# Optimization experiments

Hardware: AMD Instinct MI355X
Metric: run time of the kernel (lower is better)

Reference implementation:

```python
import jax, jax.numpy as jnp
import numpy as np

B, C, H, W = 8, 64, 96, 320
K = 50
HEAD = 256
CLS = 3
CIN3 = C + 2 + CLS  # feat + 2 coord maps + one-hot class


def _conv(x, w, b, pad):
    y = jax.lax.conv_general_dilated(x, w, (1, 1), [(pad, pad), (pad, pad)],
                                     dimension_numbers=('NCHW', 'OIHW', 'NCHW'))
    return y + b[None, :, None, None]


def _head2(x, w1, b1, w2, b2):
    # Conv3x3 -> ReLU -> Conv1x1 (heatmap / offset_2d / size_2d heads)
    return _conv(jax.nn.relu(_conv(x, w1, b1, 1)), w2, b2, 0)


def _head3(x, w1, b1, g, be, m, v, w2, b2):
    # Conv3x3 -> BN(eval) -> ReLU -> AdaptiveAvgPool2d(1) -> Conv1x1, returns [N, cout]
    y = _conv(x, w1, b1, 1)
    y = (y - m[None, :, None, None]) * (g * jax.lax.rsqrt(v + 1e-5))[None, :, None, None] + be[None, :, None, None]
    y = jax.nn.relu(y).mean((2, 3))
    return y @ w2.reshape(w2.shape[0], -1).T + b2


def _nms(heat):
    hmax = jax.lax.reduce_window(heat, -jnp.inf, jax.lax.max, (1, 1, 3, 3), (1, 1, 1, 1), 'SAME')
    return jnp.where(hmax == heat, heat, 0.0)


def _roi_align(feat, boxes, out=7, sr=2):
    # torchvision roi_align semantics (spatial_scale=1, aligned=False, sampling_ratio=2);
    # boxes are treated as constants w.r.t. gradients (as in torchvision).
    boxes = jax.lax.stop_gradient(boxes)
    b = boxes[:, 0].astype(jnp.int32)
    x1, y1, x2, y2 = boxes[:, 1], boxes[:, 2], boxes[:, 3], boxes[:, 4]
    bw = jnp.maximum(x2 - x1, 1.0) / out
    bh = jnp.maximum(y2 - y1, 1.0) / out
    g = (jnp.arange(out * sr, dtype=feat.dtype) + 0.5) / sr  # sample positions in bin units
    ys = y1[:, None] + g[None, :] * bh[:, None]  # [N, S]
    xs = x1[:, None] + g[None, :] * bw[:, None]
    Hf, Wf = feat.shape[2], feat.shape[3]
    def prep(c, dim):
        valid = (c >= -1.0) & (c <= dim)
        c = jnp.clip(c, 0.0, dim - 1.0)
        i0 = jnp.floor(c).astype(jnp.int32)
        i1 = jnp.minimum(i0 + 1, dim - 1)
        return i0, i1, c - i0, valid
    y0, y1i, fy, vy = prep(ys, Hf)
    x0, x1i, fx, vx = prep(xs, Wf)
    bb = b[:, None, None]
    def gather(yi, xi):
        return feat[bb, :, yi[:, :, None], xi[:, None, :]]  # [N, S, S, C]
    w00 = ((1 - fy)[:, :, None] * (1 - fx)[:, None, :])[..., None]
    w01 = ((1 - fy)[:, :, None] * fx[:, None, :])[..., None]
    w10 = (fy[:, :, None] * (1 - fx)[:, None, :])[..., None]
    w11 = (fy[:, :, None] * fx[:, None, :])[..., None]
    val = gather(y0, x0) * w00 + gather(y0, x1i) * w01 + gather(y1i, x0) * w10 + gather(y1i, x1i) * w11
    val = val * (vy[:, :, None] & vx[:, None, :])[..., None].astype(feat.dtype)
    N = boxes.shape[0]
    val = val.reshape(N, out, sr, out, sr, -1).mean((2, 4))  # avg over sampling grid
    return val.transpose(0, 3, 1, 2)  # [N, C, 7, 7]


def _project2rect(calib, p):
    f_u, f_v = calib[:, 0, 0], calib[:, 1, 1]
    c_u, c_v = calib[:, 0, 2], calib[:, 1, 2]
    b_x = calib[:, 0, 3] / -f_u
    b_y = calib[:, 1, 3] / -f_v
    x = (p[:, 0] - c_u) * p[:, 2] / f_u + b_x
    y = (p[:, 1] - c_v) * p[:, 2] / f_v + b_y
    return jnp.stack([x, y, p[:, 2]], -1)


def reference(feat, coord_ranges, calibs, mean_size, hm_w1, hm_b1, hm_w2, hm_b2, o2_w1, o2_b1, o2_w2, o2_b2, s2_w1, s2_b1, s2_w2, s2_b2, dep_w1, dep_b1, dep_g, dep_be, dep_m, dep_v, dep_w2, dep_b2, o3_w1, o3_b1, o3_g, o3_be, o3_m, o3_v, o3_w2, o3_b2, s3_w1, s3_b1, s3_g, s3_be, s3_m, s3_v, s3_w2, s3_b2, hd_w1, hd_b1, hd_g, hd_be, hd_m, hd_v, hd_w2, hd_b2):
    # dense 2D heads
    heatmap = _head2(feat, hm_w1, hm_b1, hm_w2, hm_b2)        # [B,1,H,W]
    offset_2d = _head2(feat, o2_w1, o2_b1, o2_w2, o2_b2)      # [B,2,H,W]
    size_2d = _head2(feat, s2_w1, s2_b1, s2_w2, s2_b2)        # [B,2,H,W]
    # test-mode: NMS + topK (single-class heatmap -> cls ids all 0)
    heat = _nms(jnp.clip(jax.nn.sigmoid(heatmap), 1e-4, 1.0 - 1e-4))
    _, inds = jax.lax.top_k(heat.reshape(B, -1), K)           # [B,K]
    cls_flat = jnp.zeros((B * K,), jnp.int32)
    # box2d maps in feature coords
    xg = jnp.arange(W, dtype=feat.dtype)
    yg = jnp.arange(H, dtype=feat.dtype)
    coord_map = jnp.stack([jnp.broadcast_to(xg[None, :], (H, W)), jnp.broadcast_to(yg[:, None], (H, W))], 0)
    centre = coord_map[None] + offset_2d
    box2d = jnp.concatenate([centre - size_2d / 2, centre + size_2d / 2], 1)  # [B,4,H,W]
    bidx = jnp.broadcast_to(jnp.arange(B, dtype=feat.dtype)[:, None, None, None], (B, 1, H, W))
    bm = jnp.concatenate([bidx, box2d], 1).reshape(B, 5, H * W)
    boxes = jnp.take_along_axis(bm, inds[:, None, :], 2).transpose(0, 2, 1).reshape(B * K, 5)
    roi = _roi_align(feat, boxes)                             # [N,64,7,7]
    bsel = boxes[:, 0].astype(jnp.int32)
    cr = coord_ranges[bsel]
    sx = cr[:, 1, 0] - cr[:, 0, 0]
    sy = cr[:, 1, 1] - cr[:, 0, 1]
    boxes_r = jnp.stack([boxes[:, 0],
                         boxes[:, 1] / W * sx + cr[:, 0, 0],
                         boxes[:, 2] / H * sy + cr[:, 0, 1],
                         boxes[:, 3] / W * sx + cr[:, 0, 0],
                         boxes[:, 4] / H * sy + cr[:, 0, 1]], -1)
    roi_calibs = calibs[bsel]
    ones = jnp.ones((B * K, 1), feat.dtype)
    p1 = _project2rect(roi_calibs, jnp.concatenate([boxes_r[:, 1:3], ones], -1))[:, :2]
    p2 = _project2rect(roi_calibs, jnp.concatenate([boxes_r[:, 3:5], ones], -1))[:, :2]
    cam = jnp.concatenate([p1, p2], -1)                       # [N,4]
    t = jnp.arange(7, dtype=feat.dtype) / 6.0
    xs7 = cam[:, 0:1] + t[None, :] * (cam[:, 2:3] - cam[:, 0:1])
    ys7 = cam[:, 1:2] + t[None, :] * (cam[:, 3:4] - cam[:, 1:2])
    cmx = jnp.broadcast_to(xs7[:, None, None, :], (B * K, 1, 7, 7))
    cmy = jnp.broadcast_to(ys7[:, None, :, None], (B * K, 1, 7, 7))
    hots = jax.nn.one_hot(cls_flat, CLS, dtype=feat.dtype)
    roi_full = jnp.concatenate([roi, cmx, cmy, jnp.broadcast_to(hots[:, :, None, None], (B * K, CLS, 7, 7))], 1)
    h2d = jnp.maximum(boxes_r[:, 4] - boxes_r[:, 2], 1.0)
    s3 = _head3(roi_full, s3_w1, s3_b1, s3_g, s3_be, s3_m, s3_v, s3_w2, s3_b2)  # [N,4]
    h3d_log_std = s3[:, 3:4]
    size3d_offset = s3[:, :3]
    size_3d = mean_size[cls_flat] + size3d_offset
    f_u = roi_calibs[:, 0, 0]
    depth_geo = size_3d[:, 0] / h2d * f_u
    dno = _head3(roi_full, dep_w1, dep_b1, dep_g, dep_be, dep_m, dep_v, dep_w2, dep_b2)  # [N,2]
    geo_log_std = (h3d_log_std[:, 0] + 2.0 * (jnp.log(f_u) - jnp.log(h2d)))[:, None]
    net_log_std = jax.nn.logsumexp(jnp.concatenate([dno[:, 1:2], geo_log_std], -1), -1, keepdims=True)
    depth = jnp.concatenate([1.0 / (jax.nn.sigmoid(dno[:, 0:1]) + 1e-6) - 1.0 + depth_geo[:, None], net_log_std], -1)
    heading = _head3(roi_full, hd_w1, hd_b1, hd_g, hd_be, hd_m, hd_v, hd_w2, hd_b2)
    offset_3d = _head3(roi_full, o3_w1, o3_b1, o3_g, o3_be, o3_m, o3_v, o3_w2, o3_b2)
    return (heatmap, offset_2d, size_2d, heading, depth, offset_3d, size3d_offset, h3d_log_std)


def setup_inputs() -> dict:
    keys = iter(jax.random.split(jax.random.key(0), 40))
    def rn(shape, s=0.05):
        return jax.random.normal(next(keys), shape, jnp.float32) * s
    d = {}
    d['feat'] = jax.random.normal(next(keys), (B, C, H, W), jnp.float32)
    d['coord_ranges'] = jnp.tile(jnp.array([[0.0, 0.0], [1280.0, 384.0]], jnp.float32)[None], (B, 1, 1))
    d['calibs'] = jnp.tile(jnp.array([[720.0, 0.0, 640.0, 0.04], [0.0, 720.0, 190.0, 0.01], [0.0, 0.0, 1.0, 0.003]], jnp.float32)[None], (B, 1, 1))
    d['mean_size'] = jnp.array([[1.52, 1.63, 3.88], [1.73, 0.67, 0.88], [1.77, 0.60, 1.76]], jnp.float32)
    for pfx, cout in [('hm', 1), ('o2', 2), ('s2', 2)]:
        d[pfx + '_w1'] = rn((HEAD, C, 3, 3))
        d[pfx + '_b1'] = jnp.zeros((HEAD,), jnp.float32)
        d[pfx + '_w2'] = rn((cout, HEAD, 1, 1))
        d[pfx + '_b2'] = jnp.full((cout,), -2.19, jnp.float32) if pfx == 'hm' else jnp.zeros((cout,), jnp.float32)
    for pfx, cout in [('dep', 2), ('o3', 2), ('s3', 4), ('hd', 24)]:
        d[pfx + '_w1'] = rn((HEAD, CIN3, 3, 3))
        d[pfx + '_b1'] = jnp.zeros((HEAD,), jnp.float32)
        d[pfx + '_g'] = jnp.ones((HEAD,), jnp.float32)
        d[pfx + '_be'] = jnp.zeros((HEAD,), jnp.float32)
        d[pfx + '_m'] = jnp.zeros((HEAD,), jnp.float32)
        d[pfx + '_v'] = jnp.ones((HEAD,), jnp.float32)
        d[pfx + '_w2'] = rn((cout, HEAD, 1, 1))
        d[pfx + '_b2'] = jnp.zeros((cout,), jnp.float32)
    return d
```

## Files before the change

kernel.cpp:

```cpp
#include <hip/hip_runtime.h>


constexpr int OFF_O2    = 245760;
constexpr int OFF_S2    = 737280;
constexpr int OFF_HEAD  = 1228800;
constexpr int OFF_DEPTH = 1238400;
constexpr int OFF_O3D   = 1239200;
constexpr int OFF_S3D   = 1240000;
constexpr int OFF_H3D   = 1241200;

constexpr int WS_W1T  = 0;
constexpr int WS_BNSC = 635904;
constexpr int WS_BNSH = 636928;
constexpr int WS_KEEP = 637952;
constexpr int WS_INDS = 883712;
constexpr int WS_BOX  = 884112;
constexpr int WS_XS7  = 885712;
constexpr int WS_YS7  = 888512;
constexpr int WS_FU   = 891312;
constexpr int WS_H2D  = 891712;
constexpr int WS_DNO  = 892112;
constexpr int WS_ROIF = 892912;
constexpr int WS_SIG  = WS_ROIF;
constexpr int WS_W1R  = 2245312;
constexpr int WS_WPACK2 = 2245312;
constexpr int WS_FEATH  = 2540224;
constexpr int WS_FEATL  = 10618560;
constexpr long long FAST_REQ_BYTES = 18696896LL * 4;
constexpr int WS_WPACK3 = 18696896;
constexpr int WS_A3     = 19139264;
constexpr long long FAST3_REQ_BYTES = 20694464LL * 4;

typedef __attribute__((ext_vector_type(4))) float f32x4;
typedef __attribute__((ext_vector_type(8))) _Float16 f16x8;
typedef __attribute__((ext_vector_type(4))) unsigned int u32x4;

__global__ void repack_kernel(
    const float* __restrict__ w2h, const float* __restrict__ w2o, const float* __restrict__ w2s,
    const float* __restrict__ w3d, const float* __restrict__ w3o, const float* __restrict__ w3s, const float* __restrict__ w3h,
    const float* __restrict__ g0, const float* __restrict__ be0, const float* __restrict__ m0, const float* __restrict__ v0,
    const float* __restrict__ g1, const float* __restrict__ be1, const float* __restrict__ m1, const float* __restrict__ v1,
    const float* __restrict__ g2, const float* __restrict__ be2, const float* __restrict__ m2, const float* __restrict__ v2,
    const float* __restrict__ g3, const float* __restrict__ be3, const float* __restrict__ m3, const float* __restrict__ v3,
    int skip2, int skip3, float* __restrict__ ws)
{
  int i = blockIdx.x * 256 + threadIdx.x;
  if (i < 3 * 147456) {
    if (skip2) return;
    int br = i / 147456, r = i - br * 147456, q = r >> 8, c = r & 255;
    const float* src = br == 0 ? w2h : (br == 1 ? w2o : w2s);
    ws[WS_W1R + i] = src[c * 576 + q];
  } else if (i < 3 * 147456 + 4 * 158976) {
    if (skip3) return;
    int j = i - 3 * 147456;
    int br = j / 158976, r = j - br * 158976, q = r >> 8, c = r & 255;
    const float* src = br == 0 ? w3d : (br == 1 ? w3o : (br == 2 ? w3s : w3h));
    ws[WS_W1T + j] = src[c * 621 + q];
  } else {
    int j = i - (3 * 147456 + 4 * 158976);
    if (j < 1024) {
      int br = j >> 8, c = j & 255;
      const float* g  = br == 0 ? g0  : (br == 1 ? g1  : (br == 2 ? g2  : g3));
      const float* be = br == 0 ? be0 : (br == 1 ? be1 : (br == 2 ? be2 : be3));
      const float* m  = br == 0 ? m0  : (br == 1 ? m1  : (br == 2 ? m2  : m3));
      const float* v  = br == 0 ? v0  : (br == 1 ? v1  : (br == 2 ? v2  : v3));
      float sc = g[c] * rsqrtf(v[c] + 1e-5f);
      ws[WS_BNSC + j] = sc;
      ws[WS_BNSH + j] = be[c] - m[c] * sc;
    }
  }
}

__global__ void wpack2_kernel(const float* __restrict__ hm_w1, const float* __restrict__ o2_w1,
                              const float* __restrict__ s2_w1, float* __restrict__ ws)
{
  int i = blockIdx.x * 256 + threadIdx.x;
  if (i >= 4 * 18 * 256 * 32) return;
  int br = i / 147456; int r = i - br * 147456;
  int c = r / 8192; int r2 = r - c * 8192;
  int n = r2 >> 5; int kk = r2 & 31;
  int kg = c * 32 + kk;
  int tap = kg >> 6, ci = kg & 63;
  const float* w1 = (br == 0) ? o2_w1 : (br == 1 ? s2_w1 : hm_w1);
  float v = w1[n * 576 + ci * 9 + tap];
  _Float16 hi = (_Float16)v;
  _Float16 valh;
  if (br == 3) valh = (_Float16)(v - (float)hi);
  else valh = hi;
  unsigned short bits = __builtin_bit_cast(unsigned short, valh);
  long long didx = (((((long long)br * 18 + c) * 16 + (n >> 4)) * 4 + (kk >> 3)) * 128) + (n & 15) * 8 + (kk & 7);
  unsigned short* dst = (unsigned short*)(ws + WS_WPACK2);
  dst[didx] = bits;
}

__global__ void wpack3_kernel(const float* __restrict__ w3d, const float* __restrict__ w3o,
                              const float* __restrict__ w3s, const float* __restrict__ w3h,
                              float* __restrict__ ws)
{
  int i = blockIdx.x * 256 + threadIdx.x;
  if (i >= 4 * 27 * 256 * 32) return;
  int br = i / 221184; int r = i - br * 221184;
  int s = r / 8192; int r2 = r - s * 8192;
  int n = r2 >> 5; int kk = r2 & 31;
  int tap = s / 3; int cc = s - tap * 3;
  int ch = cc * 32 + kk;
  const float* w1 = br == 0 ? w3d : (br == 1 ? w3o : (br == 2 ? w3s : w3h));
  float v = (ch < 69) ? w1[n * 621 + ch * 9 + tap] : 0.f;
  unsigned short bits = __builtin_bit_cast(unsigned short, (_Float16)v);
  long long didx = (((((long long)br * 27 + s) * 16 + (n >> 4)) * 4 + (kk >> 3)) * 128) + (n & 15) * 8 + (kk & 7);
  ((unsigned short*)(ws + WS_WPACK3))[didx] = bits;
}

__global__ void pad_zero_kernel(float* __restrict__ ws)
{
  int i = blockIdx.x * 256 + threadIdx.x;
  if (i >= 428032) return;
  int arr = i / 214016; int r = i - arr * 214016;
  int px = r >> 5, q = r & 31;
  int b = px / 836, pr = px - b * 836;
  int yy, xx;
  if (pr < 322) { yy = 0; xx = pr; }
  else if (pr < 644) { yy = 97; xx = pr - 322; }
  else { int t = pr - 644; yy = 1 + (t >> 1); xx = (t & 1) * 321; }
  unsigned int* dst = (unsigned int*)(ws + (arr ? WS_FEATL : WS_FEATH));
  dst[((b * 98 + yy) * 322 + xx) * 32 + q] = 0u;
}

__global__ __launch_bounds__(256) void transpose_kernel(const float* __restrict__ feat, float* __restrict__ ws)
{
  __shared__ unsigned short T2[2][64 * 65];
  int bx = blockIdx.x;
  int b = bx / 480; int r = bx % 480; int y = r / 5; int x0 = (r % 5) * 64;
  int tid = threadIdx.x;
  int lx = tid & 63, grp = tid >> 6;
  #pragma unroll
  for (int it = 0; it < 16; ++it) {
    int ci = it * 4 + grp;
    float v = feat[(((b * 64 + ci) * 96 + y) * 320) + x0 + lx];
    _Float16 h = (_Float16)v;
    _Float16 l = (_Float16)(v - (float)h);
    T2[0][lx * 65 + ci] = __builtin_bit_cast(unsigned short, h);
    T2[1][lx * 65 + ci] = __builtin_bit_cast(unsigned short, l);
  }
  __syncthreads();
  unsigned int* fH = (unsigned int*)(ws + WS_FEATH);
  unsigned int* fL = (unsigned int*)(ws + WS_FEATL);
  #pragma unroll
  for (int it = 0; it < 16; ++it) {
    int unit = it * 256 + tid;
    int arr = unit >> 11; int un = unit & 2047;
    int x = un >> 5, pr = un & 31;
    unsigned int lo = T2[arr][x * 65 + pr * 2];
    unsigned int hi = T2[arr][x * 65 + pr * 2 + 1];
    unsigned int val = lo | (hi << 16);
    unsigned int* dst = arr ? fL : fH;
    dst[((b * 98 + y + 1) * 322 + (x0 + x + 1)) * 32 + pr] = val;
  }
}


__global__ __launch_bounds__(256, 2) void head2_os_kernel(
    const float* __restrict__ ws,
    const float* __restrict__ b1o, const float* __restrict__ b1s,
    const float* __restrict__ w2o, const float* __restrict__ w2s,
    const float* __restrict__ b2o, const float* __restrict__ b2s,
    float* __restrict__ out)
{
  __shared__ unsigned char tile[4 * 8 * 66 * 16];
  __shared__ float red[1024];
  const int tid = threadIdx.x;
  const int l = tid & 63, w = tid >> 6;
  const int bx = blockIdx.x;
  const int b = bx / 240; int r = bx % 240;
  const int y0 = (r / 5) * 2; const int x0 = (r % 5) * 64;
  const unsigned short* fH = (const unsigned short*)(ws + WS_FEATH) + (size_t)b * (98 * 322 * 64);
  const _Float16* wpk = (const _Float16*)(ws + WS_WPACK2);

  for (int t = 0; t < 9; ++t) {
    int u = t * 256 + tid;
    if (u < 2112) {
      int row = u / 528; int rem = u - row * 528;
      int j0 = rem / 66, x = rem - j0 * 66;
      u32x4 v = *(const u32x4*)(fH + ((y0 + row) * 322 + (x0 + x)) * 64 + j0 * 8);
      *(u32x4*)(tile + ((row * 8 + j0) * 66 + x) * 16) = v;
    }
  }
  __syncthreads();

  const int l15 = l & 15, lg = l >> 4;
  const int aBase = (lg * 66 + l15) * 16;

  #pragma unroll 1
  for (int br = 0; br < 2; ++br) {
    f32x4 acc[8][4];
    #pragma unroll
    for (int i = 0; i < 8; ++i)
      #pragma unroll
      for (int j = 0; j < 4; ++j) acc[i][j] = (f32x4)(0.f);

    const _Float16* wB = wpk + (((long long)(br * 18) * 16 + w * 4) * 4 + lg) * 128 + l15 * 8;

    #pragma unroll
    for (int s = 0; s < 18; ++s) {
      const int tap = s >> 1, half = s & 1;
      const int ky = tap / 3, kx = tap - ky * 3;
      const int stepOff = ((ky * 8 + half * 4) * 66 + kx) * 16;
      f16x8 af[8], bf[4];
      #pragma unroll
      for (int pf = 0; pf < 8; ++pf) {
        const int frOff = (pf < 4) ? pf * 256 : 8448 + (pf - 4) * 256;
        af[pf] = *(const f16x8*)(tile + aBase + frOff + stepOff);
      }
      #pragma unroll
      for (int nf = 0; nf < 4; ++nf)
        bf[nf] = *(const f16x8*)(wB + s * 8192 + nf * 512);
      #pragma unroll
      for (int pf = 0; pf < 8; ++pf)
        #pragma unroll
        for (int nf = 0; nf < 4; ++nf)
          acc[pf][nf] = __builtin_amdgcn_mfma_f32_16x16x32_f16(af[pf], bf[nf], acc[pf][nf], 0, 0, 0);
    }

    const float* b1 = br == 0 ? b1o : b1s;
    const float* w2 = br == 0 ? w2o : w2s;
    const float* b2 = br == 0 ? b2o : b2s;
    float b1v_[4], w2v[2][4];
    #pragma unroll
    for (int nf = 0; nf < 4; ++nf) {
      int n = w * 64 + nf * 16 + l15;
      b1v_[nf] = b1[n];
      w2v[0][nf] = w2[n];
      w2v[1][nf] = w2[256 + n];
    }
    __syncthreads();
    #pragma unroll
    for (int pf = 0; pf < 8; ++pf) {
      #pragma unroll
      for (int rr = 0; rr < 4; ++rr) {
        float s0 = 0.f, s1 = 0.f;
        #pragma unroll
        for (int nf = 0; nf < 4; ++nf) {
          float yv = acc[pf][nf][rr] + b1v_[nf];
          yv = yv > 0.f ? yv : 0.f;
          s0 = fmaf(w2v[0][nf], yv, s0);
          s1 = fmaf(w2v[1][nf], yv, s1);
        }
        #pragma unroll
        for (int m = 1; m < 16; m <<= 1) {
          s0 += __shfl_xor(s0, m);
          s1 += __shfl_xor(s1, m);
        }
        if (l15 == 0) {
          int p = pf * 16 + lg * 4 + rr;
          red[(w * 2 + 0) * 128 + p] = s0;
          red[(w * 2 + 1) * 128 + p] = s1;
        }
      }
    }
    __syncthreads();
    {
      int p = tid & 127, o = tid >> 7;
      float s = red[(0 * 2 + o) * 128 + p] + red[(1 * 2 + o) * 128 + p] +
                red[(2 * 2 + o) * 128 + p] + red[(3 * 2 + o) * 128 + p] + b2[o];
      int ypix = y0 + (p >> 6), xpix = x0 + (p & 63);
      int base = (br == 0) ? OFF_O2 : OFF_S2;
      out[base + ((b * 2 + o) * 96 + ypix) * 320 + xpix] = s;
    }
  }
}

__global__ __launch_bounds__(256, 2) void head2_hm_kernel(
    const float* __restrict__ ws,
    const float* __restrict__ b1h, const float* __restrict__ w2h, const float* __restrict__ b2h,
    float* __restrict__ out)
{
  __shared__ unsigned char tiles[2 * 3 * 8 * 66 * 16];
  __shared__ float red[256];
  const int tid = threadIdx.x;
  const int l = tid & 63, w = tid >> 6;
  const int bx = blockIdx.x;
  const int b = bx / 480; int r = bx % 480;
  const int y = r / 5; const int x0 = (r % 5) * 64;
  const unsigned short* fH = (const unsigned short*)(ws + WS_FEATH) + (size_t)b * (98 * 322 * 64);
  const unsigned short* fL = (const unsigned short*)(ws + WS_FEATL) + (size_t)b * (98 * 322 * 64);
  const _Float16* wpk = (const _Float16*)(ws + WS_WPACK2);

  for (int t = 0; t < 13; ++t) {
    int u = t * 256 + tid;
    if (u < 3168) {
      int arr = u >= 1584; int uu = u - arr * 1584;
      int row = uu / 528; int rem = uu - row * 528;
      int j0 = rem / 66, x = rem - j0 * 66;
      const unsigned short* src = arr ? fL : fH;
      u32x4 v = *(const u32x4*)(src + ((y + row) * 322 + (x0 + x)) * 64 + j0 * 8);
      *(u32x4*)(tiles + arr * 25344 + ((row * 8 + j0) * 66 + x) * 16) = v;
    }
  }
  __syncthreads();

  const int l15 = l & 15, lg = l >> 4;
  const int aBase = (lg * 66 + l15) * 16;

  f32x4 acc[4][4];
  #pragma unroll
  for (int i = 0; i < 4; ++i)
    #pragma unroll
    for (int j = 0; j < 4; ++j) acc[i][j] = (f32x4)(0.f);

  const _Float16* wBH = wpk + (((long long)(2 * 18) * 16 + w * 4) * 4 + lg) * 128 + l15 * 8;
  const _Float16* wBL = wpk + (((long long)(3 * 18) * 16 + w * 4) * 4 + lg) * 128 + l15 * 8;

  #pragma unroll
  for (int s = 0; s < 18; ++s) {
    const int tap = s >> 1, half = s & 1;
    const int ky = tap / 3, kx = tap - ky * 3;
    const int stepOff = ((ky * 8 + half * 4) * 66 + kx) * 16;
    f16x8 ah[4], al[4], bh[4], bl[4];
    #pragma unroll
    for (int pf = 0; pf < 4; ++pf) {
      ah[pf] = *(const f16x8*)(tiles + aBase + pf * 256 + stepOff);
      al[pf] = *(const f16x8*)(tiles + 25344 + aBase + pf * 256 + stepOff);
    }
    #pragma unroll
    for (int nf = 0; nf < 4; ++nf) {
      bh[nf] = *(const f16x8*)(wBH + s * 8192 + nf * 512);
      bl[nf] = *(const f16x8*)(wBL + s * 8192 + nf * 512);
    }
    #pragma unroll
    for (int pf = 0; pf < 4; ++pf)
      #pragma unroll
      for (int nf = 0; nf < 4; ++nf)
        acc[pf][nf] = __builtin_amdgcn_mfma_f32_16x16x32_f16(ah[pf], bh[nf], acc[pf][nf], 0, 0, 0);
    #pragma unroll
    for (int pf = 0; pf < 4; ++pf)
      #pragma unroll
      for (int nf = 0; nf < 4; ++nf)
        acc[pf][nf] = __builtin_amdgcn_mfma_f32_16x16x32_f16(ah[pf], bl[nf], acc[pf][nf], 0, 0, 0);
    #pragma unroll
    for (int pf = 0; pf < 4; ++pf)
      #pragma unroll
      for (int nf = 0; nf < 4; ++nf)
        acc[pf][nf] = __builtin_amdgcn_mfma_f32_16x16x32_f16(al[pf], bh[nf], acc[pf][nf], 0, 0, 0);
  }

  float b1v_[4], w2v[4];
  #pragma unroll
  for (int nf = 0; nf < 4; ++nf) {
    int n = w * 64 + nf * 16 + l15;
    b1v_[nf] = b1h[n];
    w2v[nf] = w2h[n];
  }
  __syncthreads();
  #pragma unroll
  for (int pf = 0; pf < 4; ++pf) {
    #pragma unroll
    for (int rr = 0; rr < 4; ++rr) {
      float s0 = 0.f;
      #pragma unroll
      for (int nf = 0; nf < 4; ++nf) {
        float yv = acc[pf][nf][rr] + b1v_[nf];
        yv = yv > 0.f ? yv : 0.f;
        s0 = fmaf(w2v[nf], yv, s0);
      }
      #pragma unroll
      for (int m = 1; m < 16; m <<= 1) s0 += __shfl_xor(s0, m);
      if (l15 == 0) red[w * 64 + pf * 16 + lg * 4 + rr] = s0;
    }
  }
  __syncthreads();
  if (tid < 64) {
    float s = red[tid] + red[64 + tid] + red[128 + tid] + red[192 + tid] + b2h[0];
    out[(b * 96 + y) * 320 + x0 + tid] = s;
  }
}

__global__ __launch_bounds__(256) void head2_kernel(
    const float* __restrict__ feat, const float* __restrict__ ws,
    const float* __restrict__ b1h, const float* __restrict__ b1o, const float* __restrict__ b1s,
    const float* __restrict__ w2h, const float* __restrict__ w2o, const float* __restrict__ w2s,
    const float* __restrict__ b2h, const float* __restrict__ b2o, const float* __restrict__ b2s,
    float* __restrict__ out)
{
  __shared__ float xs[32 * 10 * 34];
  const int tid = threadIdx.x;
  const int tx = tid & 31, ty = tid >> 5;
  const int x0 = blockIdx.x * 32, y0 = blockIdx.y * 8, bz = blockIdx.z;
  const int px = x0 + tx, py = y0 + ty;
  const float* w1r = ws + WS_W1R;

  #pragma unroll 1
  for (int br = 0; br < 3; ++br) {
    const float* wr = w1r + br * 147456;
    const float* b1 = br == 0 ? b1h : (br == 1 ? b1o : b1s);
    const float* w2 = br == 0 ? w2h : (br == 1 ? w2o : w2s);
    const int cout = (br == 0) ? 1 : 2;
    float acc0 = 0.f, acc1 = 0.f;
    #pragma unroll 1
    for (int c0 = 0; c0 < 256; c0 += 64) {
      float part[64];
      #pragma unroll
      for (int j = 0; j < 64; ++j) part[j] = 0.f;
      #pragma unroll 1
      for (int cc = 0; cc < 2; ++cc) {
        for (int i = tid; i < 32 * 10 * 34; i += 256) {
          int ci = i / 340; int rr = i - ci * 340; int ry = rr / 34; int rx = rr - ry * 34;
          int gy = y0 + ry - 1, gx = x0 + rx - 1;
          float v = 0.f;
          if ((unsigned)gy < 96u && (unsigned)gx < 320u)
            v = feat[((bz * 64 + cc * 32 + ci) * 96 + gy) * 320 + gx];
          xs[i] = v;
        }
        __syncthreads();
        #pragma unroll 1
        for (int ci = 0; ci < 32; ++ci) {
          const float* wp = wr + ((cc * 32 + ci) * 9) * 256 + c0;
          const float* xb = &xs[ci * 340 + ty * 34 + tx];
          #pragma unroll
          for (int k = 0; k < 9; ++k) {
            float xv = xb[(k / 3) * 34 + (k % 3)];
            const float* wk = wp + k * 256;
            #pragma unroll
            for (int j = 0; j < 64; ++j) part[j] = fmaf(wk[j], xv, part[j]);
          }
        }
        __syncthreads();
      }
      #pragma unroll
      for (int j = 0; j < 64; ++j) {
        float yv = part[j] + b1[c0 + j];
        yv = yv > 0.f ? yv : 0.f;
        acc0 = fmaf(w2[c0 + j], yv, acc0);
        if (cout > 1) acc1 = fmaf(w2[256 + c0 + j], yv, acc1);
      }
    }
    if (br == 0) {
      out[(bz * 96 + py) * 320 + px] = acc0 + b2h[0];
    } else if (br == 1) {
      out[OFF_O2 + ((bz * 2 + 0) * 96 + py) * 320 + px] = acc0 + b2o[0];
      out[OFF_O2 + ((bz * 2 + 1) * 96 + py) * 320 + px] = acc1 + b2o[1];
    } else {
      out[OFF_S2 + ((bz * 2 + 0) * 96 + py) * 320 + px] = acc0 + b2s[0];
      out[OFF_S2 + ((bz * 2 + 1) * 96 + py) * 320 + px] = acc1 + b2s[1];
    }
  }
}

__global__ void nms_sig_kernel(const float* __restrict__ out, float* __restrict__ sig)
{
  int i = blockIdx.x * 256 + threadIdx.x;
  if (i >= 8 * 30720) return;
  float s = 1.f / (1.f + expf(-out[i]));
  s = s < 1e-4f ? 1e-4f : s;
  float hi = 1.f - 1e-4f;
  sig[i] = s > hi ? hi : s;
}

__global__ void nms_max_kernel(const float* __restrict__ sig, float* __restrict__ keep)
{
  int i = blockIdx.x * 256 + threadIdx.x;
  if (i >= 8 * 30720) return;
  int b = i / 30720; int r = i - b * 30720; int y = r / 320; int x = r - y * 320;
  const float* sb = sig + b * 30720;
  float v = sb[y * 320 + x];
  float m = v;
  for (int dy = -1; dy <= 1; ++dy)
    for (int dx = -1; dx <= 1; ++dx) {
      int yy = y + dy, xx = x + dx;
      if (yy >= 0 && yy < 96 && xx >= 0 && xx < 320) m = fmaxf(m, sb[yy * 320 + xx]);
    }
  keep[i] = (m == v) ? v : 0.f;
}

__global__ __launch_bounds__(256) void topk_kernel(float* ws)
{
  constexpr int CAP = 6144;
  __shared__ float cv[CAP];
  __shared__ int   cix[CAP];
  __shared__ int   cnt;
  __shared__ float wv_[4];
  __shared__ int   wi_[4];
  __shared__ int   wsl[4];
  int b = blockIdx.x, tid = threadIdx.x;
  int lane = tid & 63, wid = tid >> 6;
  if (tid == 0) cnt = 0;
  __syncthreads();
  const float* kb = ws + WS_KEEP + b * 30720;
  for (int i = tid; i < 30720; i += 256) {
    float v = kb[i];
    if (v > 0.f) {
      int pos = atomicAdd(&cnt, 1);
      if (pos < CAP) { cv[pos] = v; cix[pos] = i; }
    }
  }
  __syncthreads();
  int ncand = cnt < CAP ? cnt : CAP;
  int* inds = (int*)(ws + WS_INDS);
  for (int k = 0; k < 50; ++k) {
    float bv = -1.f; int bi = 0x7fffffff; int bs = -1;
    for (int i = tid; i < ncand; i += 256) {
      float v = cv[i]; int id = cix[i];
      if (v > bv || (v == bv && id < bi)) { bv = v; bi = id; bs = i; }
    }
    #pragma unroll
    for (int m = 1; m < 64; m <<= 1) {
      float ov = __shfl_xor(bv, m);
      int oi = __shfl_xor(bi, m);
      int os_ = __shfl_xor(bs, m);
      if (ov > bv || (ov == bv && oi < bi)) { bv = ov; bi = oi; bs = os_; }
    }
    if (lane == 0) { wv_[wid] = bv; wi_[wid] = bi; wsl[wid] = bs; }
    __syncthreads();
    if (tid == 0) {
      float fv = wv_[0]; int fi = wi_[0]; int fs = wsl[0];
      #pragma unroll
      for (int t = 1; t < 4; ++t) {
        if (wv_[t] > fv || (wv_[t] == fv && wi_[t] < fi)) { fv = wv_[t]; fi = wi_[t]; fs = wsl[t]; }
      }
      inds[b * 50 + k] = fi;
      if (fs >= 0) cv[fs] = -1.f;
    }
    __syncthreads();
  }
}

__global__ void boxes_kernel(const float* __restrict__ out, const float* __restrict__ coord_ranges,
                             const float* __restrict__ calibs, float* ws)
{
  int n = blockIdx.x * 256 + threadIdx.x;
  if (n >= 400) return;
  const int* inds = (const int*)(ws + WS_INDS);
  int b = n / 50;
  int idx = inds[n];
  int iy = idx / 320, ix = idx - iy * 320;
  float o2x = out[OFF_O2 + ((b * 2 + 0) * 96 + iy) * 320 + ix];
  float o2y = out[OFF_O2 + ((b * 2 + 1) * 96 + iy) * 320 + ix];
  float sw  = out[OFF_S2 + ((b * 2 + 0) * 96 + iy) * 320 + ix];
  float sh  = out[OFF_S2 + ((b * 2 + 1) * 96 + iy) * 320 + ix];
  float cx = (float)ix + o2x, cy = (float)iy + o2y;
  float x1 = cx - sw * 0.5f, y1 = cy - sh * 0.5f, x2 = cx + sw * 0.5f, y2 = cy + sh * 0.5f;
  ws[WS_BOX + n * 4 + 0] = x1; ws[WS_BOX + n * 4 + 1] = y1;
  ws[WS_BOX + n * 4 + 2] = x2; ws[WS_BOX + n * 4 + 3] = y2;
  float cr00 = coord_ranges[b * 4 + 0], cr01 = coord_ranges[b * 4 + 1];
  float sx = coord_ranges[b * 4 + 2] - cr00, sy = coord_ranges[b * 4 + 3] - cr01;
  float x1r = x1 / 320.f * sx + cr00, y1r = y1 / 96.f * sy + cr01;
  float x2r = x2 / 320.f * sx + cr00, y2r = y2 / 96.f * sy + cr01;
  const float* cl = calibs + b * 12;
  float fu = cl[0], cu = cl[2], bx = cl[3] / (-fu);
  float fv = cl[5], cvv = cl[6], by = cl[7] / (-fv);
  float p1x = (x1r - cu) / fu + bx, p1y = (y1r - cvv) / fv + by;
  float p2x = (x2r - cu) / fu + bx, p2y = (y2r - cvv) / fv + by;
  #pragma unroll
  for (int j = 0; j < 7; ++j) {
    float t = (float)j / 6.f;
    ws[WS_XS7 + n * 7 + j] = p1x + t * (p2x - p1x);
    ws[WS_YS7 + n * 7 + j] = p1y + t * (p2y - p1y);
  }
  ws[WS_FU + n] = fu;
  ws[WS_H2D + n] = fmaxf(y2r - y1r, 1.f);
}

__global__ __launch_bounds__(256) void roi_kernel(const float* __restrict__ feat, float* ws)
{
  int n = blockIdx.x;
  int tid = threadIdx.x;
  __shared__ int   iy0[14], iy1[14], ix0[14], ix1[14];
  __shared__ float fy[14], fx[14], vy[14], vx[14];
  float bx1 = ws[WS_BOX + n * 4], by1 = ws[WS_BOX + n * 4 + 1];
  float bx2 = ws[WS_BOX + n * 4 + 2], by2 = ws[WS_BOX + n * 4 + 3];
  if (tid < 14) {
    float bh = fmaxf(by2 - by1, 1.f) / 7.f;
    float g = ((float)tid + 0.5f) * 0.5f;
    float c = by1 + g * bh;
    vy[tid] = (c >= -1.f && c <= 96.f) ? 1.f : 0.f;
    c = fminf(fmaxf(c, 0.f), 95.f);
    int i0 = (int)floorf(c);
    iy0[tid] = i0; iy1[tid] = (i0 + 1 < 95) ? i0 + 1 : 95;
    fy[tid] = c - (float)i0;
  } else if (tid < 28) {
    int t = tid - 14;
    float bw = fmaxf(bx2 - bx1, 1.f) / 7.f;
    float g = ((float)t + 0.5f) * 0.5f;
    float c = bx1 + g * bw;
    vx[t] = (c >= -1.f && c <= 320.f) ? 1.f : 0.f;
    c = fminf(fmaxf(c, 0.f), 319.f);
    int i0 = (int)floorf(c);
    ix0[t] = i0; ix1[t] = (i0 + 1 < 319) ? i0 + 1 : 319;
    fx[t] = c - (float)i0;
  }
  __syncthreads();
  int bsel = n / 50;
  const float* fbase = feat + bsel * 64 * 30720;
  float* rf = ws + WS_ROIF + n * 3381;
  for (int i = tid; i < 64 * 49; i += 256) {
    int c = i / 49, p = i - c * 49;
    int oy = p / 7, ox = p - oy * 7;
    const float* fb = fbase + c * 30720;
    float s = 0.f;
    #pragma unroll
    for (int sy2 = 0; sy2 < 2; ++sy2) {
      #pragma unroll
      for (int sx2 = 0; sx2 < 2; ++sx2) {
        int jy = oy * 2 + sy2, jx = ox * 2 + sx2;
        const float* r0 = fb + iy0[jy] * 320;
        const float* r1 = fb + iy1[jy] * 320;
        float gy = fy[jy], gx = fx[jx];
        float v00 = r0[ix0[jx]], v01 = r0[ix1[jx]], v10 = r1[ix0[jx]], v11 = r1[ix1[jx]];
        float v = v00 * (1.f - gy) * (1.f - gx) + v01 * (1.f - gy) * gx
                + v10 * gy * (1.f - gx) + v11 * gy * gx;
        s += v * vy[jy] * vx[jx];
      }
    }
    rf[c * 49 + p] = s * 0.25f;
  }
  if (tid < 5 * 49) {
    int ch = tid / 49, p = tid - ch * 49;
    int oy = p / 7, ox = p - oy * 7;
    float v;
    if (ch == 0) v = ws[WS_XS7 + n * 7 + ox];
    else if (ch == 1) v = ws[WS_YS7 + n * 7 + oy];
    else if (ch == 2) v = 1.f;
    else v = 0.f;
    rf[(64 + ch) * 49 + p] = v;
  }
}

__global__ void roi16_kernel(float* __restrict__ ws)
{
  int n = blockIdx.x;
  const float* rf = ws + WS_ROIF + n * 3381;
  unsigned short* a3 = (unsigned short*)(ws + WS_A3) + (size_t)n * 7776;
  for (int t = 0; t < 31; ++t) {
    int i = t * 256 + threadIdx.x;
    if (i < 7776) {
      int pr = i / 96, ch = i - pr * 96;
      int py = pr / 9, px = pr - py * 9;
      float v = 0.f;
      if (py >= 1 && py <= 7 && px >= 1 && px <= 7 && ch < 69)
        v = rf[ch * 49 + (py - 1) * 7 + (px - 1)];
      a3[i] = __builtin_bit_cast(unsigned short, (_Float16)v);
    }
  }
}

__global__ __launch_bounds__(256, 2) void head3m_kernel(
    float* __restrict__ ws,
    const float* __restrict__ b1d, const float* __restrict__ b1o3, const float* __restrict__ b1s3, const float* __restrict__ b1hd,
    const float* __restrict__ w2d, const float* __restrict__ w2o3, const float* __restrict__ w2s3, const float* __restrict__ w2hd,
    const float* __restrict__ b2d, const float* __restrict__ b2o3, const float* __restrict__ b2s3, const float* __restrict__ b2hd,
    float* __restrict__ out)
{
  __shared__ unsigned char A[81 * 104 * 2];
  __shared__ float ym[256];
  const int tid = threadIdx.x;
  const int l = tid & 63, w = tid >> 6;
  const int l15 = l & 15, lg = l >> 4;
  const int n = blockIdx.x;
  const unsigned short* a3 = (const unsigned short*)(ws + WS_A3) + (size_t)n * 7776;
  const _Float16* wp3 = (const _Float16*)(ws + WS_WPACK3);

  #pragma unroll
  for (int t = 0; t < 4; ++t) {
    int u = t * 256 + tid;
    if (u < 972) {
      int row = u / 12, cu = u - row * 12;
      u32x4 v = *(const u32x4*)(a3 + u * 8);
      *(u32x4*)(A + (row * 104 + cu * 8) * 2) = v;
    }
  }
  __syncthreads();

  int aB[4];
  #pragma unroll
  for (int pf = 0; pf < 4; ++pf) {
    int p = pf * 16 + l15;
    int rb = (p < 49) ? ((p / 7) * 9 + (p % 7)) : 0;
    aB[pf] = rb * 208 + lg * 16;
  }

  #pragma unroll 1
  for (int br = 0; br < 4; ++br) {
    const float* b1 = br == 0 ? b1d : (br == 1 ? b1o3 : (br == 2 ? b1s3 : b1hd));
    const float* w2 = br == 0 ? w2d : (br == 1 ? w2o3 : (br == 2 ? w2s3 : w2hd));
    const float* b2 = br == 0 ? b2d : (br == 1 ? b2o3 : (br == 2 ? b2s3 : b2hd));
    const int cout = br == 0 ? 2 : (br == 1 ? 2 : (br == 2 ? 4 : 24));

    f32x4 acc[4][4];
    #pragma unroll
    for (int i = 0; i < 4; ++i)
      #pragma unroll
      for (int j = 0; j < 4; ++j) acc[i][j] = (f32x4)(0.f);

    const _Float16* wB3 = wp3 + (((long long)(br * 27) * 16 + w * 4) * 4 + lg) * 128 + l15 * 8;

    #pragma unroll
    for (int s = 0; s < 27; ++s) {
      const int tap = s / 3, cc = s - tap * 3;
      const int ky = tap / 3, kx = tap - ky * 3;
      const int stepOff = (ky * 9 + kx) * 208 + cc * 64;
      f16x8 af[4], bf[4];
      #pragma unroll
      for (int pf = 0; pf < 4; ++pf)
        af[pf] = *(const f16x8*)(A + aB[pf] + stepOff);
      #pragma unroll
      for (int nf = 0; nf < 4; ++nf)
        bf[nf] = *(const f16x8*)(wB3 + s * 8192 + nf * 512);
      #pragma unroll
      for (int pf = 0; pf < 4; ++pf)
        #pragma unroll
        for (int nf = 0; nf < 4; ++nf)
          acc[pf][nf] = __builtin_amdgcn_mfma_f32_16x16x32_f16(af[pf], bf[nf], acc[pf][nf], 0, 0, 0);
    }

    #pragma unroll
    for (int nf = 0; nf < 4; ++nf) {
      int nn = w * 64 + nf * 16 + l15;
      float b1n = b1[nn];
      float scn = ws[WS_BNSC + br * 256 + nn];
      float shn = ws[WS_BNSH + br * 256 + nn];
      float local = 0.f;
      #pragma unroll
      for (int pf = 0; pf < 4; ++pf) {
        #pragma unroll
        for (int rr = 0; rr < 4; ++rr) {
          int p = pf * 16 + lg * 4 + rr;
          float yv = (acc[pf][nf][rr] + b1n) * scn + shn;
          yv = yv > 0.f ? yv : 0.f;
          local += (p < 49) ? yv : 0.f;
        }
      }
      local += __shfl_xor(local, 16);
      local += __shfl_xor(local, 32);
      if (lg == 0) ym[nn] = local;
    }
    __syncthreads();
    for (int o = w; o < cout; o += 4) {
      float p = 0.f;
      #pragma unroll
      for (int t = 0; t < 4; ++t) p = fmaf(w2[o * 256 + t * 64 + l], ym[t * 64 + l], p);
      p *= (1.f / 49.f);
      #pragma unroll
      for (int off = 32; off > 0; off >>= 1) p += __shfl_down(p, off);
      if (l == 0) {
        float v = p + b2[o];
        if (br == 0) ws[WS_DNO + n * 2 + o] = v;
        else if (br == 1) out[OFF_O3D + n * 2 + o] = v;
        else if (br == 2) { if (o < 3) out[OFF_S3D + n * 3 + o] = v; else out[OFF_H3D + n] = v; }
        else out[OFF_HEAD + n * 24 + o] = v;
      }
    }
    __syncthreads();
  }
}

__global__ __launch_bounds__(256) void head3_kernel(
    float* ws,
    const float* __restrict__ b1d, const float* __restrict__ b1o3, const float* __restrict__ b1s3, const float* __restrict__ b1hd,
    const float* __restrict__ w2d, const float* __restrict__ w2o3, const float* __restrict__ w2s3, const float* __restrict__ w2hd,
    const float* __restrict__ b2d, const float* __restrict__ b2o3, const float* __restrict__ b2s3, const float* __restrict__ b2hd,
    float* __restrict__ out)
{
  int n = blockIdx.x, br = blockIdx.y;
  int c = threadIdx.x;
  __shared__ float ym[256];
  const float* wt = ws + WS_W1T + br * 158976;
  const float* b1 = br == 0 ? b1d : (br == 1 ? b1o3 : (br == 2 ? b1s3 : b1hd));
  const float* w2 = br == 0 ? w2d : (br == 1 ? w2o3 : (br == 2 ? w2s3 : w2hd));
  const float* b2 = br == 0 ? b2d : (br == 1 ? b2o3 : (br == 2 ? b2s3 : b2hd));
  const int cout = br == 0 ? 2 : (br == 1 ? 2 : (br == 2 ? 4 : 24));
  const float* xin0 = ws + WS_ROIF + n * 3381;

  float acc[49];
  #pragma unroll
  for (int i = 0; i < 49; ++i) acc[i] = 0.f;

  #pragma unroll 1
  for (int ci = 0; ci < 69; ++ci) {
    float wv[9];
    #pragma unroll
    for (int k = 0; k < 9; ++k) wv[k] = wt[(ci * 9 + k) * 256 + c];
    const float* xin = xin0 + ci * 49;
    #pragma unroll
    for (int y = 0; y < 7; ++y) {
      float xr[9];
      xr[0] = 0.f; xr[8] = 0.f;
      #pragma unroll
      for (int q = 0; q < 7; ++q) xr[q + 1] = xin[y * 7 + q];
      #pragma unroll
      for (int ky = 0; ky < 3; ++ky) {
        int pyy = y + 1 - ky;
        if (pyy >= 0 && pyy < 7) {
          #pragma unroll
          for (int kx = 0; kx < 3; ++kx) {
            float w = wv[ky * 3 + kx];
            #pragma unroll
            for (int pxx = 0; pxx < 7; ++pxx)
              acc[pyy * 7 + pxx] = fmaf(w, xr[pxx + kx], acc[pyy * 7 + pxx]);
          }
        }
      }
    }
  }
  float b1c = b1[c];
  float sc = ws[WS_BNSC + br * 256 + c];
  float sh = ws[WS_BNSH + br * 256 + c];
  float sum = 0.f;
  #pragma unroll
  for (int i = 0; i < 49; ++i) {
    float yv = (acc[i] + b1c) * sc + sh;
    sum += yv > 0.f ? yv : 0.f;
  }
  ym[c] = sum / 49.f;
  __syncthreads();
  int lane = c & 63, wid = c >> 6;
  for (int o = wid; o < cout; o += 4) {
    float p = 0.f;
    #pragma unroll
    for (int t = 0; t < 4; ++t) p = fmaf(w2[o * 256 + t * 64 + lane], ym[t * 64 + lane], p);
    #pragma unroll
    for (int off = 32; off > 0; off >>= 1) p += __shfl_down(p, off);
    if (lane == 0) {
      float v = p + b2[o];
      if (br == 0) ws[WS_DNO + n * 2 + o] = v;
      else if (br == 1) out[OFF_O3D + n * 2 + o] = v;
      else if (br == 2) { if (o < 3) out[OFF_S3D + n * 3 + o] = v; else out[OFF_H3D + n] = v; }
      else out[OFF_HEAD + n * 24 + o] = v;
    }
  }
}

__global__ void depth_kernel(const float* ws, const float* __restrict__ mean_size, float* __restrict__ out)
{
  int n = blockIdx.x * 256 + threadIdx.x;
  if (n >= 400) return;
  float h3d = out[OFF_H3D + n];
  float s30 = out[OFF_S3D + n * 3];
  float size0 = mean_size[0] + s30;
  float f = ws[WS_FU + n], h = ws[WS_H2D + n];
  float dgeo = size0 / h * f;
  float geo = h3d + 2.f * (logf(f) - logf(h));
  float a = ws[WS_DNO + n * 2 + 1];
  float mx = fmaxf(a, geo);
  float nls = mx + logf(expf(a - mx) + expf(geo - mx));
  float sg = 1.f / (1.f + expf(-ws[WS_DNO + n * 2]));
  out[OFF_DEPTH + n * 2] = 1.f / (sg + 1e-6f) - 1.f + dgeo;
  out[OFF_DEPTH + n * 2 + 1] = nls;
}

extern "C" void kernel_launch(void* const* d_in, const int* in_sizes, int n_in,
                              void* d_out, int out_size, void* d_ws, size_t ws_size,
                              hipStream_t stream)
{
  const float* feat         = (const float*)d_in[0];
  const float* coord_ranges = (const float*)d_in[1];
  const float* calibs       = (const float*)d_in[2];
  const float* mean_size    = (const float*)d_in[3];
  const float* hm_w1 = (const float*)d_in[4];
  const float* hm_b1 = (const float*)d_in[5];
  const float* hm_w2 = (const float*)d_in[6];
  const float* hm_b2 = (const float*)d_in[7];
  const float* o2_w1 = (const float*)d_in[8];
  const float* o2_b1 = (const float*)d_in[9];
  const float* o2_w2 = (const float*)d_in[10];
  const float* o2_b2 = (const float*)d_in[11];
  const float* s2_w1 = (const float*)d_in[12];
  const float* s2_b1 = (const float*)d_in[13];
  const float* s2_w2 = (const float*)d_in[14];
  const float* s2_b2 = (const float*)d_in[15];
  const float* dep_w1 = (const float*)d_in[16];
  const float* dep_b1 = (const float*)d_in[17];
  const float* dep_g  = (const float*)d_in[18];
  const float* dep_be = (const float*)d_in[19];
  const float* dep_m  = (const float*)d_in[20];
  const float* dep_v  = (const float*)d_in[21];
  const float* dep_w2 = (const float*)d_in[22];
  const float* dep_b2 = (const float*)d_in[23];
  const float* o3_w1 = (const float*)d_in[24];
  const float* o3_b1 = (const float*)d_in[25];
  const float* o3_g  = (const float*)d_in[26];
  const float* o3_be = (const float*)d_in[27];
  const float* o3_m  = (const float*)d_in[28];
  const float* o3_v  = (const float*)d_in[29];
  const float* o3_w2 = (const float*)d_in[30];
  const float* o3_b2 = (const float*)d_in[31];
  const float* s3_w1 = (const float*)d_in[32];
  const float* s3_b1 = (const float*)d_in[33];
  const float* s3_g  = (const float*)d_in[34];
  const float* s3_be = (const float*)d_in[35];
  const float* s3_m  = (const float*)d_in[36];
  const float* s3_v  = (const float*)d_in[37];
  const float* s3_w2 = (const float*)d_in[38];
  const float* s3_b2 = (const float*)d_in[39];
  const float* hd_w1 = (const float*)d_in[40];
  const float* hd_b1 = (const float*)d_in[41];
  const float* hd_g  = (const float*)d_in[42];
  const float* hd_be = (const float*)d_in[43];
  const float* hd_m  = (const float*)d_in[44];
  const float* hd_v  = (const float*)d_in[45];
  const float* hd_w2 = (const float*)d_in[46];
  const float* hd_b2 = (const float*)d_in[47];

  float* out = (float*)d_out;
  float* ws  = (float*)d_ws;
  bool fast  = (long long)ws_size >= FAST_REQ_BYTES;
  bool fast3 = (long long)ws_size >= FAST3_REQ_BYTES;

  repack_kernel<<<dim3((3 * 147456 + 4 * 158976 + 1024 + 255) / 256), 256, 0, stream>>>(
      hm_w1, o2_w1, s2_w1, dep_w1, o3_w1, s3_w1, hd_w1,
      dep_g, dep_be, dep_m, dep_v, o3_g, o3_be, o3_m, o3_v,
      s3_g, s3_be, s3_m, s3_v, hd_g, hd_be, hd_m, hd_v,
      fast ? 1 : 0, fast3 ? 1 : 0, ws);

  if (fast) {
    wpack2_kernel<<<dim3((4 * 18 * 256 * 32 + 255) / 256), 256, 0, stream>>>(hm_w1, o2_w1, s2_w1, ws);
    pad_zero_kernel<<<dim3((428032 + 255) / 256), 256, 0, stream>>>(ws);
    transpose_kernel<<<dim3(3840), 256, 0, stream>>>(feat, ws);
    head2_os_kernel<<<dim3(1920), 256, 0, stream>>>(ws, o2_b1, s2_b1, o2_w2, s2_w2, o2_b2, s2_b2, out);
    head2_hm_kernel<<<dim3(3840), 256, 0, stream>>>(ws, hm_b1, hm_w2, hm_b2, out);
  } else {
    head2_kernel<<<dim3(10, 12, 8), 256, 0, stream>>>(feat, ws,
        hm_b1, o2_b1, s2_b1, hm_w2, o2_w2, s2_w2, hm_b2, o2_b2, s2_b2, out);
  }
  if (fast3)
    wpack3_kernel<<<dim3((4 * 27 * 256 * 32 + 255) / 256), 256, 0, stream>>>(dep_w1, o3_w1, s3_w1, hd_w1, ws);

  nms_sig_kernel<<<dim3(960), 256, 0, stream>>>(out, ws + WS_SIG);
  nms_max_kernel<<<dim3(960), 256, 0, stream>>>(ws + WS_SIG, ws + WS_KEEP);
  topk_kernel<<<dim3(8), 256, 0, stream>>>(ws);
  boxes_kernel<<<dim3(2), 256, 0, stream>>>(out, coord_ranges, calibs, ws);
  roi_kernel<<<dim3(400), 256, 0, stream>>>(feat, ws);
  if (fast3) {
    roi16_kernel<<<dim3(400), 256, 0, stream>>>(ws);
    head3m_kernel<<<dim3(400), 256, 0, stream>>>(ws,
        dep_b1, o3_b1, s3_b1, hd_b1, dep_w2, o3_w2, s3_w2, hd_w2,
        dep_b2, o3_b2, s3_b2, hd_b2, out);
  } else {
    head3_kernel<<<dim3(400, 4), 256, 0, stream>>>(ws,
        dep_b1, o3_b1, s3_b1, hd_b1, dep_w2, o3_w2, s3_w2, hd_w2,
        dep_b2, o3_b2, s3_b2, hd_b2, out);
  }
  depth_kernel<<<dim3(2), 256, 0, stream>>>(ws, mean_size, out);
}
```

Baseline: 623.4 us.

## Swizzle head2 LDS tiles, pipeline operand loads, fuse sigmoid and roi16 into producers

The heatmap head kernel now stores its feature tile in an XOR-swizzled LDS layout to cut bank conflicts, and double-buffers A/B fragment loads across steps. It also computes the clamped sigmoid in its epilogue, so the separate nms_sig launch is skipped. The offset/size head now processes one row per block instead of two, using fewer accumulator registers but reusing weights less. The fp16 ROI packing is folded into roi_kernel, removing one launch and a global round trip.

```diff
diff --git a/kernel.cpp b/kernel.cpp
--- a/kernel.cpp
+++ b/kernel.cpp
@@ -158,6 +158,9 @@
   }
 }
 
+__device__ __forceinline__ int tile_off_sw(int row, int x, int j) {
+  return ((row * 66 + x) * 8 + (j ^ (x & 7))) * 16;
+}
 
 __global__ __launch_bounds__(256, 2) void head2_os_kernel(
     const float* __restrict__ ws,
@@ -166,22 +169,22 @@
     const float* __restrict__ b2o, const float* __restrict__ b2s,
     float* __restrict__ out)
 {
-  __shared__ unsigned char tile[4 * 8 * 66 * 16];
-  __shared__ float red[1024];
+  __shared__ unsigned char tile[3 * 8 * 66 * 16];
+  __shared__ float red[512];
   const int tid = threadIdx.x;
   const int l = tid & 63, w = tid >> 6;
   const int bx = blockIdx.x;
-  const int b = bx / 240; int r = bx % 240;
-  const int y0 = (r / 5) * 2; const int x0 = (r % 5) * 64;
+  const int b = bx / 480; int r = bx % 480;
+  const int y = r / 5; const int x0 = (r % 5) * 64;
   const unsigned short* fH = (const unsigned short*)(ws + WS_FEATH) + (size_t)b * (98 * 322 * 64);
   const _Float16* wpk = (const _Float16*)(ws + WS_WPACK2);
 
-  for (int t = 0; t < 9; ++t) {
+  for (int t = 0; t < 7; ++t) {
     int u = t * 256 + tid;
-    if (u < 2112) {
+    if (u < 1584) {
       int row = u / 528; int rem = u - row * 528;
-      int j0 = rem / 66, x = rem - j0 * 66;
-      u32x4 v = *(const u32x4*)(fH + ((y0 + row) * 322 + (x0 + x)) * 64 + j0 * 8);
+      int x = rem >> 3, j0 = rem & 7;
+      u32x4 v = *(const u32x4*)(fH + ((y + row) * 322 + (x0 + x)) * 64 + j0 * 8);
       *(u32x4*)(tile + ((row * 8 + j0) * 66 + x) * 16) = v;
     }
   }
@@ -192,9 +195,9 @@
 
   #pragma unroll 1
   for (int br = 0; br < 2; ++br) {
-    f32x4 acc[8][4];
-    #pragma unroll
-    for (int i = 0; i < 8; ++i)
+    f32x4 acc[4][4];
+    #pragma unroll
+    for (int i = 0; i < 4; ++i)
       #pragma unroll
       for (int j = 0; j < 4; ++j) acc[i][j] = (f32x4)(0.f);
 
@@ -205,17 +208,15 @@
       const int tap = s >> 1, half = s & 1;
       const int ky = tap / 3, kx = tap - ky * 3;
       const int stepOff = ((ky * 8 + half * 4) * 66 + kx) * 16;
-      f16x8 af[8], bf[4];
-      #pragma unroll
-      for (int pf = 0; pf < 8; ++pf) {
-        const int frOff = (pf < 4) ? pf * 256 : 8448 + (pf - 4) * 256;
-        af[pf] = *(const f16x8*)(tile + aBase + frOff + stepOff);
-      }
+      f16x8 af[4], bf[4];
+      #pragma unroll
+      for (int pf = 0; pf < 4; ++pf)
+        af[pf] = *(const f16x8*)(tile + aBase + pf * 256 + stepOff);
       #pragma unroll
       for (int nf = 0; nf < 4; ++nf)
         bf[nf] = *(const f16x8*)(wB + s * 8192 + nf * 512);
       #pragma unroll
-      for (int pf = 0; pf < 8; ++pf)
+      for (int pf = 0; pf < 4; ++pf)
         #pragma unroll
         for (int nf = 0; nf < 4; ++nf)
           acc[pf][nf] = __builtin_amdgcn_mfma_f32_16x16x32_f16(af[pf], bf[nf], acc[pf][nf], 0, 0, 0);
@@ -234,7 +235,7 @@
     }
     __syncthreads();
     #pragma unroll
-    for (int pf = 0; pf < 8; ++pf) {
+    for (int pf = 0; pf < 4; ++pf) {
       #pragma unroll
       for (int rr = 0; rr < 4; ++rr) {
         float s0 = 0.f, s1 = 0.f;
@@ -252,19 +253,18 @@
         }
         if (l15 == 0) {
           int p = pf * 16 + lg * 4 + rr;
-          red[(w * 2 + 0) * 128 + p] = s0;
-          red[(w * 2 + 1) * 128 + p] = s1;
+          red[(w * 2 + 0) * 64 + p] = s0;
+          red[(w * 2 + 1) * 64 + p] = s1;
         }
       }
     }
     __syncthreads();
-    {
-      int p = tid & 127, o = tid >> 7;
-      float s = red[(0 * 2 + o) * 128 + p] + red[(1 * 2 + o) * 128 + p] +
-                red[(2 * 2 + o) * 128 + p] + red[(3 * 2 + o) * 128 + p] + b2[o];
-      int ypix = y0 + (p >> 6), xpix = x0 + (p & 63);
+    if (tid < 128) {
+      int p = tid & 63, o = tid >> 6;
+      float s = red[(0 * 2 + o) * 64 + p] + red[(1 * 2 + o) * 64 + p] +
+                red[(2 * 2 + o) * 64 + p] + red[(3 * 2 + o) * 64 + p] + b2[o];
       int base = (br == 0) ? OFF_O2 : OFF_S2;
-      out[base + ((b * 2 + o) * 96 + ypix) * 320 + xpix] = s;
+      out[base + ((b * 2 + o) * 96 + y) * 320 + x0 + p] = s;
     }
   }
 }
@@ -272,9 +272,9 @@
 __global__ __launch_bounds__(256, 2) void head2_hm_kernel(
     const float* __restrict__ ws,
     const float* __restrict__ b1h, const float* __restrict__ w2h, const float* __restrict__ b2h,
-    float* __restrict__ out)
-{
-  __shared__ unsigned char tiles[2 * 3 * 8 * 66 * 16];
+    float* __restrict__ out, float* __restrict__ sig)
+{
+  __shared__ unsigned short tiles[2][3 * 66 * 64];
   __shared__ float red[256];
   const int tid = threadIdx.x;
   const int l = tid & 63, w = tid >> 6;
@@ -290,16 +290,15 @@
     if (u < 3168) {
       int arr = u >= 1584; int uu = u - arr * 1584;
       int row = uu / 528; int rem = uu - row * 528;
-      int j0 = rem / 66, x = rem - j0 * 66;
+      int x = rem >> 3, j0 = rem & 7;
       const unsigned short* src = arr ? fL : fH;
       u32x4 v = *(const u32x4*)(src + ((y + row) * 322 + (x0 + x)) * 64 + j0 * 8);
-      *(u32x4*)(tiles + arr * 25344 + ((row * 8 + j0) * 66 + x) * 16) = v;
+      *(u32x4*)((char*)&tiles[arr][0] + tile_off_sw(row, x, j0)) = v;
     }
   }
   __syncthreads();
 
   const int l15 = l & 15, lg = l >> 4;
-  const int aBase = (lg * 66 + l15) * 16;
 
   f32x4 acc[4][4];
   #pragma unroll
@@ -307,25 +306,28 @@
     #pragma unroll
     for (int j = 0; j < 4; ++j) acc[i][j] = (f32x4)(0.f);
 
-  const _Float16* wBH = wpk + (((long long)(2 * 18) * 16 + w * 4) * 4 + lg) * 128 + l15 * 8;
-  const _Float16* wBL = wpk + (((long long)(3 * 18) * 16 + w * 4) * 4 + lg) * 128 + l15 * 8;
-
-  #pragma unroll
-  for (int s = 0; s < 18; ++s) {
-    const int tap = s >> 1, half = s & 1;
-    const int ky = tap / 3, kx = tap - ky * 3;
-    const int stepOff = ((ky * 8 + half * 4) * 66 + kx) * 16;
-    f16x8 ah[4], al[4], bh[4], bl[4];
+  f16x8 AH0[4], AL0[4], AH1[4], AL1[4];
+  f16x8 BH0[4], BL0[4], BH1[4], BL1[4];
+
+  auto ldA = [&](f16x8* ah, f16x8* al, int s) {
+    int tap = s >> 1, half = s & 1;
+    int ky = tap / 3, kx = tap - ky * 3;
     #pragma unroll
     for (int pf = 0; pf < 4; ++pf) {
-      ah[pf] = *(const f16x8*)(tiles + aBase + pf * 256 + stepOff);
-      al[pf] = *(const f16x8*)(tiles + 25344 + aBase + pf * 256 + stepOff);
-    }
+      int p = pf * 16 + l15;
+      int off = tile_off_sw(ky, p + kx, half * 4 + lg);
+      ah[pf] = *(const f16x8*)((const char*)&tiles[0][0] + off);
+      al[pf] = *(const f16x8*)((const char*)&tiles[1][0] + off);
+    }
+  };
+  auto ldB = [&](f16x8* bh, f16x8* bl, int s) {
     #pragma unroll
     for (int nf = 0; nf < 4; ++nf) {
-      bh[nf] = *(const f16x8*)(wBH + s * 8192 + nf * 512);
-      bl[nf] = *(const f16x8*)(wBL + s * 8192 + nf * 512);
-    }
+      bh[nf] = *(const f16x8*)(wpk + (((2LL * 18 + s) * 16 + (w * 4 + nf)) * 4 + lg) * 128 + l15 * 8);
+      bl[nf] = *(const f16x8*)(wpk + (((3LL * 18 + s) * 16 + (w * 4 + nf)) * 4 + lg) * 128 + l15 * 8);
+    }
+  };
+  auto mm3 = [&](f16x8* ah, f16x8* al, f16x8* bh, f16x8* bl) {
     #pragma unroll
     for (int pf = 0; pf < 4; ++pf)
       #pragma unroll
@@ -341,6 +343,16 @@
       #pragma unroll
       for (int nf = 0; nf < 4; ++nf)
         acc[pf][nf] = __builtin_amdgcn_mfma_f32_16x16x32_f16(al[pf], bh[nf], acc[pf][nf], 0, 0, 0);
+  };
+
+  ldA(AH0, AL0, 0); ldB(BH0, BL0, 0);
+  #pragma unroll 1
+  for (int s2 = 0; s2 < 9; ++s2) {
+    const int s = s2 * 2;
+    ldA(AH1, AL1, s + 1); ldB(BH1, BL1, s + 1);
+    mm3(AH0, AL0, BH0, BL0);
+    if (s2 < 8) { ldA(AH0, AL0, s + 2); ldB(BH0, BL0, s + 2); }
+    mm3(AH1, AL1, BH1, BL1);
   }
 
   float b1v_[4], w2v[4];
@@ -370,7 +382,11 @@
   __syncthreads();
   if (tid < 64) {
     float s = red[tid] + red[64 + tid] + red[128 + tid] + red[192 + tid] + b2h[0];
-    out[(b * 96 + y) * 320 + x0 + tid] = s;
+    int idx = (b * 96 + y) * 320 + x0 + tid;
+    out[idx] = s;
+    float sg = 1.f / (1.f + expf(-s));
+    sg = fminf(fmaxf(sg, 1e-4f), 1.f - 1e-4f);
+    sig[idx] = sg;
   }
 }
 
@@ -559,7 +575,7 @@
   ws[WS_H2D + n] = fmaxf(y2r - y1r, 1.f);
 }
 
-__global__ __launch_bounds__(256) void roi_kernel(const float* __restrict__ feat, float* ws)
+__global__ __launch_bounds__(256) void roi_kernel(const float* __restrict__ feat, int fast3, float* ws)
 {
   int n = blockIdx.x;
   int tid = threadIdx.x;
@@ -622,22 +638,19 @@
     else v = 0.f;
     rf[(64 + ch) * 49 + p] = v;
   }
-}
-
-__global__ void roi16_kernel(float* __restrict__ ws)
-{
-  int n = blockIdx.x;
-  const float* rf = ws + WS_ROIF + n * 3381;
-  unsigned short* a3 = (unsigned short*)(ws + WS_A3) + (size_t)n * 7776;
-  for (int t = 0; t < 31; ++t) {
-    int i = t * 256 + threadIdx.x;
-    if (i < 7776) {
-      int pr = i / 96, ch = i - pr * 96;
-      int py = pr / 9, px = pr - py * 9;
-      float v = 0.f;
-      if (py >= 1 && py <= 7 && px >= 1 && px <= 7 && ch < 69)
-        v = rf[ch * 49 + (py - 1) * 7 + (px - 1)];
-      a3[i] = __builtin_bit_cast(unsigned short, (_Float16)v);
+  if (fast3) {
+    __syncthreads();
+    unsigned short* a3 = (unsigned short*)(ws + WS_A3) + (size_t)n * 7776;
+    for (int t = 0; t < 31; ++t) {
+      int i = t * 256 + tid;
+      if (i < 7776) {
+        int pr = i / 96, ch = i - pr * 96;
+        int py = pr / 9, px = pr - py * 9;
+        float v = 0.f;
+        if (py >= 1 && py <= 7 && px >= 1 && px <= 7 && ch < 69)
+          v = rf[ch * 49 + (py - 1) * 7 + (px - 1)];
+        a3[i] = __builtin_bit_cast(unsigned short, (_Float16)v);
+      }
     }
   }
 }
@@ -914,22 +927,21 @@
     wpack2_kernel<<<dim3((4 * 18 * 256 * 32 + 255) / 256), 256, 0, stream>>>(hm_w1, o2_w1, s2_w1, ws);
     pad_zero_kernel<<<dim3((428032 + 255) / 256), 256, 0, stream>>>(ws);
     transpose_kernel<<<dim3(3840), 256, 0, stream>>>(feat, ws);
-    head2_os_kernel<<<dim3(1920), 256, 0, stream>>>(ws, o2_b1, s2_b1, o2_w2, s2_w2, o2_b2, s2_b2, out);
-    head2_hm_kernel<<<dim3(3840), 256, 0, stream>>>(ws, hm_b1, hm_w2, hm_b2, out);
+    head2_os_kernel<<<dim3(3840), 256, 0, stream>>>(ws, o2_b1, s2_b1, o2_w2, s2_w2, o2_b2, s2_b2, out);
+    head2_hm_kernel<<<dim3(3840), 256, 0, stream>>>(ws, hm_b1, hm_w2, hm_b2, out, ws + WS_SIG);
   } else {
     head2_kernel<<<dim3(10, 12, 8), 256, 0, stream>>>(feat, ws,
         hm_b1, o2_b1, s2_b1, hm_w2, o2_w2, s2_w2, hm_b2, o2_b2, s2_b2, out);
+    nms_sig_kernel<<<dim3(960), 256, 0, stream>>>(out, ws + WS_SIG);
   }
   if (fast3)
     wpack3_kernel<<<dim3((4 * 27 * 256 * 32 + 255) / 256), 256, 0, stream>>>(dep_w1, o3_w1, s3_w1, hd_w1, ws);
 
-  nms_sig_kernel<<<dim3(960), 256, 0, stream>>>(out, ws + WS_SIG);
   nms_max_kernel<<<dim3(960), 256, 0, stream>>>(ws + WS_SIG, ws + WS_KEEP);
   topk_kernel<<<dim3(8), 256, 0, stream>>>(ws);
   boxes_kernel<<<dim3(2), 256, 0, stream>>>(out, coord_ranges, calibs, ws);
-  roi_kernel<<<dim3(400), 256, 0, stream>>>(feat, ws);
+  roi_kernel<<<dim3(400), 256, 0, stream>>>(feat, fast3 ? 1 : 0, ws);
   if (fast3) {
-    roi16_kernel<<<dim3(400), 256, 0, stream>>>(ws);
     head3m_kernel<<<dim3(400), 256, 0, stream>>>(ws,
         dep_b1, o3_b1, s3_b1, hd_b1, dep_w2, o3_w2, s3_w2, hd_w2,
         dep_b2, o3_b2, s3_b2, hd_b2, out);
```

New measurement: 585.9 us, median of 2. 6.0% less time.
